# Performance work log

Hardware: AMD Instinct MI355X
Metric: run time of the kernel (lower is better)

## Reference

```python
import jax, jax.numpy as jnp
import numpy as np

# bitsandbytes NF4 codebook (16 levels)
NF4 = jnp.array([-1.0, -0.6961928009986877, -0.5250730514526367, -0.39491748809814453,
                 -0.28444138169288635, -0.18477343022823334, -0.09105003625154495, 0.0,
                 0.07958029955625534, 0.16093020141124725, 0.24611230194568634,
                 0.33791524171829224, 0.44070982933044434, 0.5626170039176941,
                 0.7229568362236023, 1.0], dtype=jnp.float32)
BLOCK = 64  # NF4 quantization blocksize
HD, M, TOKENS = 4096, 11008, 512


def dequant_nf4(codes, absmax, out_f, in_f):
    # codes: int [out_f, in_f] in [0,16); absmax: float [out_f*in_f/BLOCK]
    w = NF4[codes.reshape(-1, BLOCK)] * absmax[:, None]
    return w.reshape(out_f, in_f)


def setup_inputs() -> dict:
    key = jax.random.key(0)
    ks = jax.random.split(key, 7)
    x = jax.random.normal(ks[0], (TOKENS, HD), dtype=jnp.float32)
    gate_codes = jax.random.randint(ks[1], (M, HD), 0, 16, dtype=jnp.int32)
    up_codes = jax.random.randint(ks[2], (M, HD), 0, 16, dtype=jnp.int32)
    down_codes = jax.random.randint(ks[3], (HD, M), 0, 16, dtype=jnp.int32)
    n_blk = (M * HD) // BLOCK
    gate_absmax = jax.random.uniform(ks[4], (n_blk,), dtype=jnp.float32) * 0.02 + 1e-3
    up_absmax = jax.random.uniform(ks[5], (n_blk,), dtype=jnp.float32) * 0.02 + 1e-3
    down_absmax = jax.random.uniform(ks[6], (n_blk,), dtype=jnp.float32) * 0.02 + 1e-3
    return {"x": x, "gate_codes": gate_codes, "gate_absmax": gate_absmax,
            "up_codes": up_codes, "up_absmax": up_absmax,
            "down_codes": down_codes, "down_absmax": down_absmax}


def reference(x, gate_codes, gate_absmax, up_codes, up_absmax, down_codes, down_absmax):
    # Dequantize NF4 weights on the fly, then SwiGLU MLP:
    # down( silu(gate(x)) * up(x) )
    Wg = dequant_nf4(gate_codes, gate_absmax, M, HD)   # [m, hd]
    Wu = dequant_nf4(up_codes, up_absmax, M, HD)       # [m, hd]
    Wd = dequant_nf4(down_codes, down_absmax, HD, M)   # [hd, m]
    g = x @ Wg.T                                       # [tokens, m]
    u = x @ Wu.T                                       # [tokens, m]
    h = jax.nn.silu(g) * u                             # [tokens, m]
    return h @ Wd.T                                    # [tokens, hd]
```

## Files before the change

kernel.cpp:

```cpp
#include <hip/hip_runtime.h>
#include <hip/hip_fp16.h>
#include <cstdint>
#include <cstddef>


using float4v = __attribute__((ext_vector_type(4))) float;
using half8   = __attribute__((ext_vector_type(8))) _Float16;

__constant__ float NF4TAB[16] = {
  -1.0f, -0.6961928009986877f, -0.5250730514526367f, -0.39491748809814453f,
  -0.28444138169288635f, -0.18477343022823334f, -0.09105003625154495f, 0.0f,
  0.07958029955625534f, 0.16093020141124725f, 0.24611230194568634f,
  0.33791524171829224f, 0.44070982933044434f, 0.5626170039176941f,
  0.7229568362236023f, 1.0f };

#define BARRIER() asm volatile("s_waitcnt lgkmcnt(0)\n\ts_barrier" ::: "memory")


template <bool ATOMIC>
__global__ __launch_bounds__(256, 2) void gemm_nf4(
    const __half* __restrict__ Apk,
    const int* __restrict__ c0, const float* __restrict__ am0,
    const int* __restrict__ c1, const float* __restrict__ am1,
    __half* __restrict__ o0, __half* __restrict__ o1,
    float* __restrict__ outF,
    int N, int K, int Kc, int Ntiles)
{
  __shared__ __half    Bb[2][64 * 72];
  __shared__ unsigned  ptab[256];

  const int tid  = threadIdx.x;
  const int lane = tid & 63;
  const int wave = tid >> 6;

  {
    __half2 pr = __floats2half2_rn(NF4TAB[tid & 15], NF4TAB[tid >> 4]);
    ptab[tid] = *(const unsigned*)&pr;
  }

  const int bid = blockIdx.x;
  const int mt  = bid & 1;
  const int r   = bid >> 1;
  const int nt  = r % Ntiles;
  const int r2  = r / Ntiles;

  const int k0 = ATOMIC ? r2 * Kc : 0;
  const int nk = Kc >> 6;
  const int* codes  = (!ATOMIC && r2) ? c1 : c0;
  const float* amax = (!ATOMIC && r2) ? am1 : am0;
  __half* outH      = (!ATOMIC && r2) ? o1 : o0;

  const int row0 = mt * 256;
  const int col0 = nt * 64;
  const int Kb   = K >> 6;

  const int bn = tid >> 2;
  const int bq = tid & 3;
  const int4* cSrc   = (const int4*)(codes + (size_t)(col0 + bn) * K + k0);
  const float* amSrc = amax + (size_t)(col0 + bn) * Kb + (k0 >> 6);

  const int kb0 = k0 >> 5;
  const int mb0 = (row0 >> 4) + wave * 4;

  float4v acc[4][4];
  {
    float4v z = {0.f, 0.f, 0.f, 0.f};
    #pragma unroll
    for (int i = 0; i < 4; ++i)
      #pragma unroll
      for (int j = 0; j < 4; ++j) acc[i][j] = z;
  }

  int4  cr[2][4];
  float amr[2];
  half8 apf[2][8];

#define LOADC(S, KT)                                                            \
  { const int4* _p = cSrc + (KT) * 16;                                          \
    cr[S][0] = _p[bq];      cr[S][1] = _p[4 + bq];                              \
    cr[S][2] = _p[8 + bq];  cr[S][3] = _p[12 + bq];                             \
    amr[S] = amSrc[KT]; }

#define DEQB(BUFI, S)                                                           \
  { const __half _ah = __float2half(amr[S]);                                    \
    const __half2 _am2 = __half2{_ah, _ah};                                     \
    _Pragma("unroll")                                                           \
    for (int _i = 0; _i < 4; ++_i) {                                            \
      unsigned _w0 = ptab[cr[S][_i].x | (cr[S][_i].y << 4)];                    \
      unsigned _w1 = ptab[cr[S][_i].z | (cr[S][_i].w << 4)];                    \
      __half2 _p0 = __hmul2(*(const __half2*)&_w0, _am2);                       \
      __half2 _p1 = __hmul2(*(const __half2*)&_w1, _am2);                       \
      uint2 _wv; _wv.x = *(const unsigned*)&_p0; _wv.y = *(const unsigned*)&_p1;\
      *(uint2*)&Bb[BUFI][bn * 72 + _i * 16 + bq * 4] = _wv; } }

#define LOADA8(DST, KT)                                                         \
  { _Pragma("unroll")                                                           \
    for (int _i = 0; _i < 4; ++_i)                                              \
      DST[_i] = *(const half8*)(Apk +                                           \
        ((size_t)((kb0 + (KT) * 2) * 32 + mb0 + _i) * 64 + lane) * 8);          \
    _Pragma("unroll")                                                           \
    for (int _i = 0; _i < 4; ++_i)                                              \
      DST[4 + _i] = *(const half8*)(Apk +                                       \
        ((size_t)((kb0 + (KT) * 2 + 1) * 32 + mb0 + _i) * 64 + lane) * 8); }

  LOADC(0, 0);
  if (nk > 1) LOADC(1, 1);
  BARRIER();
  DEQB(0, 0);
  LOADA8(apf[0], 0);
  if (nk > 2) LOADC(0, 2);
  BARRIER();

#define BODY(KT, S, NP)                                                         \
  { if ((KT) + 1 < nk) {                                                        \
      DEQB(NP, NP);                            \
      LOADA8(apf[NP], (KT) + 1);                  \
      if ((KT) + 3 < nk) LOADC(NP, (KT) + 3);               \
    }                                                                           \
    half8 bf[4];                                                                \
    _Pragma("unroll")                                                           \
    for (int _j = 0; _j < 4; ++_j)                                              \
      bf[_j] = *(const half8*)&Bb[S][(_j * 16 + (lane & 15)) * 72 + ((lane >> 4) << 3)]; \
    _Pragma("unroll")                                                           \
    for (int _i = 0; _i < 4; ++_i)                                              \
      _Pragma("unroll")                                                         \
      for (int _j = 0; _j < 4; ++_j)                                            \
        acc[_i][_j] = __builtin_amdgcn_mfma_f32_16x16x32_f16(apf[S][_i], bf[_j], acc[_i][_j], 0, 0, 0); \
    _Pragma("unroll")                                                           \
    for (int _j = 0; _j < 4; ++_j)                                              \
      bf[_j] = *(const half8*)&Bb[S][(_j * 16 + (lane & 15)) * 72 + 32 + ((lane >> 4) << 3)]; \
    _Pragma("unroll")                                                           \
    for (int _i = 0; _i < 4; ++_i)                                              \
      _Pragma("unroll")                                                         \
      for (int _j = 0; _j < 4; ++_j)                                            \
        acc[_i][_j] = __builtin_amdgcn_mfma_f32_16x16x32_f16(apf[S][4 + _i], bf[_j], acc[_i][_j], 0, 0, 0); \
    BARRIER(); }

  int kt = 0;
  while (kt + 2 <= nk) { BODY(kt, 0, 1); BODY(kt + 1, 1, 0); kt += 2; }
  if (kt < nk) BODY(kt, 0, 1);

  if (ATOMIC) {
    const int ccol0 = col0 + (lane & 15);
    const int crow0 = row0 + wave * 64 + ((lane >> 4) << 2);
    #pragma unroll
    for (int i = 0; i < 4; ++i)
      #pragma unroll
      for (int j = 0; j < 4; ++j)
        #pragma unroll
        for (int rr = 0; rr < 4; ++rr) {
          const size_t idx = (size_t)(crow0 + i * 16 + rr) * N + (ccol0 + j * 16);
          atomicAdd(&outF[idx], acc[i][j][rr]);
        }
  } else {
    const int jj    = lane & 7;
    const int lb    = (lane >> 3) & 1;
    const int rbase = (lane >> 4) << 2;
    const int kb_c  = col0 >> 5;
    #pragma unroll
    for (int i = 0; i < 4; ++i) {
      const int mb = (row0 >> 4) + wave * 4 + i;
      #pragma unroll
      for (int j = 0; j < 4; ++j) {
        const int kb = kb_c + (j >> 1);
        const int lp = ((j & 1) * 2 + lb) * 16 + rbase;
        #pragma unroll
        for (int rr = 0; rr < 4; ++rr) {
          const size_t a = ((size_t)(kb * 32 + mb) * 64 + (lp + rr)) * 8 + jj;
          outH[a] = __float2half(acc[i][j][rr]);
        }
      }
    }
  }
#undef LOADC
#undef DEQB
#undef LOADA8
#undef BODY
}

__global__ void cast_pack_kernel(const float* __restrict__ x,
                                 __half* __restrict__ xp, int nGrp) {
  int pid = blockIdx.x * blockDim.x + threadIdx.x;
  if (pid >= nGrp) return;
  const int lane = pid & 63;
  const int grp  = pid >> 6;
  const int mb   = grp & 31;
  const int kb   = grp >> 5;
  const int m = mb * 16 + (lane & 15);
  const int k = kb * 32 + ((lane >> 4) << 3);
  const float4* src = (const float4*)(x + (size_t)m * 4096 + k);
  float4 v0 = src[0], v1 = src[1];
  __half2 h0 = __floats2half2_rn(v0.x, v0.y), h1 = __floats2half2_rn(v0.z, v0.w);
  __half2 h2 = __floats2half2_rn(v1.x, v1.y), h3 = __floats2half2_rn(v1.z, v1.w);
  uint4 o;
  o.x = *(const unsigned*)&h0; o.y = *(const unsigned*)&h1;
  o.z = *(const unsigned*)&h2; o.w = *(const unsigned*)&h3;
  ((uint4*)xp)[pid] = o;
}

__global__ void swiglu_kernel(const __half* __restrict__ g,
                              const __half* __restrict__ u,
                              __half* __restrict__ h, int n2) {
  int i = blockIdx.x * blockDim.x + threadIdx.x;
  if (i < n2) {
    float2 gf = __half22float2(((const __half2*)g)[i]);
    float2 uf = __half22float2(((const __half2*)u)[i]);
    float h0 = gf.x / (1.f + __expf(-gf.x)) * uf.x;
    float h1 = gf.y / (1.f + __expf(-gf.y)) * uf.y;
    ((__half2*)h)[i] = __floats2half2_rn(h0, h1);
  }
}

extern "C" void kernel_launch(void* const* d_in, const int* in_sizes, int n_in,
                              void* d_out, int out_size, void* d_ws, size_t ws_size,
                              hipStream_t stream)
{
  (void)in_sizes; (void)n_in; (void)ws_size;
  const float* x            = (const float*)d_in[0];
  const int*   gate_codes   = (const int*)d_in[1];
  const float* gate_absmax  = (const float*)d_in[2];
  const int*   up_codes     = (const int*)d_in[3];
  const float* up_absmax    = (const float*)d_in[4];
  const int*   down_codes   = (const int*)d_in[5];
  const float* down_absmax  = (const float*)d_in[6];
  float* out = (float*)d_out;

  __half* xp = (__half*)d_ws;
  __half* g  = xp + (size_t)512 * 4096;
  __half* u  = g  + (size_t)512 * 11008;

  hipMemsetAsync(d_out, 0, (size_t)out_size * sizeof(float), stream);

  cast_pack_kernel<<<1024, 256, 0, stream>>>(x, xp, (512 * 4096) / 8);

  gemm_nf4<false><<<688, 256, 0, stream>>>(xp, gate_codes, gate_absmax,
                                           up_codes, up_absmax,
                                           g, u, nullptr,
                                           11008, 4096, 4096, 172);

  swiglu_kernel<<<11008, 256, 0, stream>>>(g, u, g, (512 * 11008) / 2);

  gemm_nf4<true><<<512, 256, 0, stream>>>(g, down_codes, down_absmax,
                                          nullptr, nullptr, nullptr, nullptr,
                                          out, 4096, 11008, 2752, 64);
}
```

Before: 657.1 us.

## Retile NF4 GEMM to full-M 512x32 tiles with XCD-aware block mapping

Each workgroup now covers all 512 token rows and a 32-wide output column slice, instead of a 256x64 tile. Every weight column is therefore dequantized exactly once rather than once per M-half, which cuts redundant global code reads and dequant work. Blocks are remapped so that neighbouring tiles land on the same XCD, the A-fragment prefetch is moved into the loop body without double buffering, and the occupancy hint is raised to 3 workgroups. In exchange each wave issues more MFMAs per B fragment and the A loads have less latency hiding.

```diff
diff --git a/kernel.cpp b/kernel.cpp
--- a/kernel.cpp
+++ b/kernel.cpp
@@ -18,7 +18,7 @@
 
 
 template <bool ATOMIC>
-__global__ __launch_bounds__(256, 2) void gemm_nf4(
+__global__ __launch_bounds__(256, 3) void gemm_nf4(
     const __half* __restrict__ Apk,
     const int* __restrict__ c0, const float* __restrict__ am0,
     const int* __restrict__ c1, const float* __restrict__ am1,
@@ -26,23 +26,32 @@
     float* __restrict__ outF,
     int N, int K, int Kc, int Ntiles)
 {
-  __shared__ __half    Bb[2][64 * 72];
+  __shared__ __half    Bb[2][32 * 80];
   __shared__ unsigned  ptab[256];
 
   const int tid  = threadIdx.x;
   const int lane = tid & 63;
   const int wave = tid >> 6;
+  const int l15  = lane & 15;
+  const int hi8  = (lane >> 4) << 3;
 
   {
     __half2 pr = __floats2half2_rn(NF4TAB[tid & 15], NF4TAB[tid >> 4]);
     ptab[tid] = *(const unsigned*)&pr;
   }
 
-  const int bid = blockIdx.x;
-  const int mt  = bid & 1;
-  const int r   = bid >> 1;
-  const int nt  = r % Ntiles;
-  const int r2  = r / Ntiles;
+  int nt, r2;
+  if (ATOMIC) {
+    const int xcd  = blockIdx.x & 7;
+    const int slot = blockIdx.x >> 3;
+    r2 = xcd >> 1;
+    nt = (xcd & 1) * (Ntiles >> 1) + slot;
+  } else {
+    const int nwg = gridDim.x;
+    const int bid = (blockIdx.x & 7) * (nwg >> 3) + (blockIdx.x >> 3);
+    nt = bid % Ntiles;
+    r2 = bid / Ntiles;
+  }
 
   const int k0 = ATOMIC ? r2 * Kc : 0;
   const int nk = Kc >> 6;
@@ -50,90 +59,87 @@
   const float* amax = (!ATOMIC && r2) ? am1 : am0;
   __half* outH      = (!ATOMIC && r2) ? o1 : o0;
 
-  const int row0 = mt * 256;
-  const int col0 = nt * 64;
+  const int col0 = nt * 32;
   const int Kb   = K >> 6;
 
-  const int bn = tid >> 2;
-  const int bq = tid & 3;
+  const int bn = tid >> 3;
+  const int bq = tid & 7;
   const int4* cSrc   = (const int4*)(codes + (size_t)(col0 + bn) * K + k0);
   const float* amSrc = amax + (size_t)(col0 + bn) * Kb + (k0 >> 6);
 
   const int kb0 = k0 >> 5;
-  const int mb0 = (row0 >> 4) + wave * 4;
-
-  float4v acc[4][4];
+  const int mb0 = wave * 8;
+  const __half* pA = Apk + (size_t)mb0 * 512 + (size_t)lane * 8;
+
+  float4v acc[8][2];
   {
     float4v z = {0.f, 0.f, 0.f, 0.f};
     #pragma unroll
-    for (int i = 0; i < 4; ++i)
+    for (int i = 0; i < 8; ++i)
       #pragma unroll
-      for (int j = 0; j < 4; ++j) acc[i][j] = z;
-  }
-
-  int4  cr[2][4];
+      for (int j = 0; j < 2; ++j) acc[i][j] = z;
+  }
+
+  int4  cr[2][2];
   float amr[2];
-  half8 apf[2][8];
+  half8 apf[8], apf2[8];
 
 #define LOADC(S, KT)                                                            \
   { const int4* _p = cSrc + (KT) * 16;                                          \
-    cr[S][0] = _p[bq];      cr[S][1] = _p[4 + bq];                              \
-    cr[S][2] = _p[8 + bq];  cr[S][3] = _p[12 + bq];                             \
+    cr[S][0] = _p[bq * 2]; cr[S][1] = _p[bq * 2 + 1];                           \
     amr[S] = amSrc[KT]; }
 
 #define DEQB(BUFI, S)                                                           \
   { const __half _ah = __float2half(amr[S]);                                    \
     const __half2 _am2 = __half2{_ah, _ah};                                     \
+    unsigned _w0 = ptab[cr[S][0].x | (cr[S][0].y << 4)];                        \
+    unsigned _w1 = ptab[cr[S][0].z | (cr[S][0].w << 4)];                        \
+    unsigned _w2 = ptab[cr[S][1].x | (cr[S][1].y << 4)];                        \
+    unsigned _w3 = ptab[cr[S][1].z | (cr[S][1].w << 4)];                        \
+    __half2 _p0 = __hmul2(*(const __half2*)&_w0, _am2);                         \
+    __half2 _p1 = __hmul2(*(const __half2*)&_w1, _am2);                         \
+    __half2 _p2 = __hmul2(*(const __half2*)&_w2, _am2);                         \
+    __half2 _p3 = __hmul2(*(const __half2*)&_w3, _am2);                         \
+    uint4 _wv;                                                                  \
+    _wv.x = *(const unsigned*)&_p0; _wv.y = *(const unsigned*)&_p1;             \
+    _wv.z = *(const unsigned*)&_p2; _wv.w = *(const unsigned*)&_p3;             \
+    *(uint4*)&Bb[BUFI][bn * 80 + bq * 8] = _wv; }
+
+#define LOADA(DST, KT, KK)                                                      \
+  { const __half* _pa = pA + ((size_t)(kb0 + (KT) * 2 + (KK)) << 14);           \
     _Pragma("unroll")                                                           \
-    for (int _i = 0; _i < 4; ++_i) {                                            \
-      unsigned _w0 = ptab[cr[S][_i].x | (cr[S][_i].y << 4)];                    \
-      unsigned _w1 = ptab[cr[S][_i].z | (cr[S][_i].w << 4)];                    \
-      __half2 _p0 = __hmul2(*(const __half2*)&_w0, _am2);                       \
-      __half2 _p1 = __hmul2(*(const __half2*)&_w1, _am2);                       \
-      uint2 _wv; _wv.x = *(const unsigned*)&_p0; _wv.y = *(const unsigned*)&_p1;\
-      *(uint2*)&Bb[BUFI][bn * 72 + _i * 16 + bq * 4] = _wv; } }
-
-#define LOADA8(DST, KT)                                                         \
+    for (int _i = 0; _i < 8; ++_i)                                              \
+      DST[_i] = *(const half8*)(_pa + _i * 512); }
+
+#define LDBF(BF, S, KK)                                                         \
   { _Pragma("unroll")                                                           \
-    for (int _i = 0; _i < 4; ++_i)                                              \
-      DST[_i] = *(const half8*)(Apk +                                           \
-        ((size_t)((kb0 + (KT) * 2) * 32 + mb0 + _i) * 64 + lane) * 8);          \
-    _Pragma("unroll")                                                           \
-    for (int _i = 0; _i < 4; ++_i)                                              \
-      DST[4 + _i] = *(const half8*)(Apk +                                       \
-        ((size_t)((kb0 + (KT) * 2 + 1) * 32 + mb0 + _i) * 64 + lane) * 8); }
+    for (int _j = 0; _j < 2; ++_j)                                              \
+      BF[_j] = *(const half8*)&Bb[S][(_j * 16 + l15) * 80 + (KK) * 32 + hi8]; }
+
+#define MFMA16(APF, BF)                                                         \
+  { _Pragma("unroll")                                                           \
+    for (int _i = 0; _i < 8; ++_i)                                              \
+      _Pragma("unroll")                                                         \
+      for (int _j = 0; _j < 2; ++_j)                                            \
+        acc[_i][_j] = __builtin_amdgcn_mfma_f32_16x16x32_f16(APF[_i], BF[_j], acc[_i][_j], 0, 0, 0); }
 
   LOADC(0, 0);
   if (nk > 1) LOADC(1, 1);
   BARRIER();
   DEQB(0, 0);
-  LOADA8(apf[0], 0);
   if (nk > 2) LOADC(0, 2);
   BARRIER();
 
 #define BODY(KT, S, NP)                                                         \
-  { if ((KT) + 1 < nk) {                                                        \
-      DEQB(NP, NP);                            \
-      LOADA8(apf[NP], (KT) + 1);                  \
-      if ((KT) + 3 < nk) LOADC(NP, (KT) + 3);               \
-    }                                                                           \
-    half8 bf[4];                                                                \
-    _Pragma("unroll")                                                           \
-    for (int _j = 0; _j < 4; ++_j)                                              \
-      bf[_j] = *(const half8*)&Bb[S][(_j * 16 + (lane & 15)) * 72 + ((lane >> 4) << 3)]; \
-    _Pragma("unroll")                                                           \
-    for (int _i = 0; _i < 4; ++_i)                                              \
-      _Pragma("unroll")                                                         \
-      for (int _j = 0; _j < 4; ++_j)                                            \
-        acc[_i][_j] = __builtin_amdgcn_mfma_f32_16x16x32_f16(apf[S][_i], bf[_j], acc[_i][_j], 0, 0, 0); \
-    _Pragma("unroll")                                                           \
-    for (int _j = 0; _j < 4; ++_j)                                              \
-      bf[_j] = *(const half8*)&Bb[S][(_j * 16 + (lane & 15)) * 72 + 32 + ((lane >> 4) << 3)]; \
-    _Pragma("unroll")                                                           \
-    for (int _i = 0; _i < 4; ++_i)                                              \
-      _Pragma("unroll")                                                         \
-      for (int _j = 0; _j < 4; ++_j)                                            \
-        acc[_i][_j] = __builtin_amdgcn_mfma_f32_16x16x32_f16(apf[S][4 + _i], bf[_j], acc[_i][_j], 0, 0, 0); \
+  { LOADA(apf, KT, 0);                                                          \
+    if ((KT) + 1 < nk) DEQB(NP, NP);                                            \
+    LOADA(apf2, KT, 1);                                                         \
+    if ((KT) + 3 < nk) LOADC(NP, (KT) + 3);                                     \
+    half8 bf[2];                                                                \
+    LDBF(bf, S, 0);                                                             \
+    MFMA16(apf, bf);                                                            \
+    LDBF(bf, S, 1);                                                             \
+    MFMA16(apf2, bf);                                                           \
     BARRIER(); }
 
   int kt = 0;
@@ -141,12 +147,12 @@
   if (kt < nk) BODY(kt, 0, 1);
 
   if (ATOMIC) {
-    const int ccol0 = col0 + (lane & 15);
-    const int crow0 = row0 + wave * 64 + ((lane >> 4) << 2);
+    const int ccol0 = col0 + l15;
+    const int crow0 = wave * 128 + ((lane >> 4) << 2);
     #pragma unroll
-    for (int i = 0; i < 4; ++i)
+    for (int i = 0; i < 8; ++i)
       #pragma unroll
-      for (int j = 0; j < 4; ++j)
+      for (int j = 0; j < 2; ++j)
         #pragma unroll
         for (int rr = 0; rr < 4; ++rr) {
           const size_t idx = (size_t)(crow0 + i * 16 + rr) * N + (ccol0 + j * 16);
@@ -156,14 +162,13 @@
     const int jj    = lane & 7;
     const int lb    = (lane >> 3) & 1;
     const int rbase = (lane >> 4) << 2;
-    const int kb_c  = col0 >> 5;
+    const int kb    = col0 >> 5;
     #pragma unroll
-    for (int i = 0; i < 4; ++i) {
-      const int mb = (row0 >> 4) + wave * 4 + i;
+    for (int i = 0; i < 8; ++i) {
+      const int mb = wave * 8 + i;
       #pragma unroll
-      for (int j = 0; j < 4; ++j) {
-        const int kb = kb_c + (j >> 1);
-        const int lp = ((j & 1) * 2 + lb) * 16 + rbase;
+      for (int j = 0; j < 2; ++j) {
+        const int lp = (j * 2 + lb) * 16 + rbase;
         #pragma unroll
         for (int rr = 0; rr < 4; ++rr) {
           const size_t a = ((size_t)(kb * 32 + mb) * 64 + (lp + rr)) * 8 + jj;
@@ -174,7 +179,9 @@
   }
 #undef LOADC
 #undef DEQB
-#undef LOADA8
+#undef LOADA
+#undef LDBF
+#undef MFMA16
 #undef BODY
 }
 
@@ -236,11 +243,11 @@
   gemm_nf4<false><<<688, 256, 0, stream>>>(xp, gate_codes, gate_absmax,
                                            up_codes, up_absmax,
                                            g, u, nullptr,
-                                           11008, 4096, 4096, 172);
+                                           11008, 4096, 4096, 344);
 
   swiglu_kernel<<<11008, 256, 0, stream>>>(g, u, g, (512 * 11008) / 2);
 
   gemm_nf4<true><<<512, 256, 0, stream>>>(g, down_codes, down_absmax,
                                           nullptr, nullptr, nullptr, nullptr,
-                                          out, 4096, 11008, 2752, 64);
-}
+                                          out, 4096, 11008, 2752, 128);
+}
```

New measurement: 684.3 us. +4.1%, slower.
